# Optimization experiments

Hardware: AMD Instinct MI355X
Metric: run time of the kernel (lower is better)

Reference implementation:

```python
import jax, jax.numpy as jnp
import numpy as np

B, T, D, K = 16, 8192, 64, 1024


def setup_inputs() -> dict:
    key = jax.random.key(0)
    k1, k2 = jax.random.split(key)
    x = jax.random.normal(k1, (B, T, D, 1), dtype=jnp.float32)
    weight = jax.random.normal(k2, (K, D), dtype=jnp.float32)
    return {"x": x, "weight": weight}


def reference(x, weight):
    # x: [B, T, D, 1] -> squeeze trailing dim -> [B, T, D]
    xs = jnp.squeeze(x, axis=-1)
    x2 = jnp.sum(xs * xs, axis=-1, keepdims=True)          # [B, T, 1]
    e2 = jnp.sum(weight * weight, axis=-1)                 # [K]
    xe = jnp.einsum('btd,kd->btk', xs, weight)             # [B, T, K]
    dist2 = x2 - 2.0 * xe + e2                             # [B, T, K]
    indices = jnp.argmin(dist2, axis=-1)                   # [B, T] int
    quantized = jnp.take(weight, indices, axis=0)          # [B, T, D]
    return quantized, indices
```

## Files before the change

kernel.cpp:

```cpp
#include <hip/hip_runtime.h>

#define MTOK  131072
#define DIMD  64
#define KCODE 1024
#define TPB   256

typedef __bf16 bf16x8 __attribute__((ext_vector_type(8)));
typedef float  f32x4  __attribute__((ext_vector_type(4)));

__device__ __forceinline__ f32x4 mfma16(bf16x8 a, bf16x8 b, f32x4 c) {
    return __builtin_amdgcn_mfma_f32_16x16x32_bf16(a, b, c, 0, 0, 0);
}

__global__ __launch_bounds__(256) void prep_kernel(
    const float* __restrict__ w, __bf16* __restrict__ wpk,
    float* __restrict__ e2n, float* __restrict__ e2) {
    int b   = blockIdx.x;
    int tid = threadIdx.x;
    if (b < 64) {
        int cb  = b;
        int win = tid >> 6, lane = tid & 63;
        int q = lane >> 4, m = lane & 15;
        int k = cb * 16 + m;
        int d0 = (win & 1) * 32 + q * 8;
        const float* src = w + (size_t)k * DIMD + d0;
        float4 v0 = *(const float4*)(src);
        float4 v1 = *(const float4*)(src + 4);
        float f[8] = {v0.x, v0.y, v0.z, v0.w, v1.x, v1.y, v1.z, v1.w};
        bf16x8 o;
#pragma unroll
        for (int j = 0; j < 8; ++j) {
            __bf16 h = (__bf16)f[j];
            o[j] = (win < 2) ? h : (__bf16)(f[j] - (float)h);
        }
        *(bf16x8*)(wpk + ((size_t)(cb * 4 + win) * 64 + lane) * 8) = o;
    } else {
        int k2 = (b - 64) * 256 + tid;
        const float4* row = (const float4*)(w + (size_t)k2 * DIMD);
        float s = 0.f;
#pragma unroll
        for (int i = 0; i < 16; ++i) {
            float4 v = row[i];
            s = fmaf(v.x, v.x, s); s = fmaf(v.y, v.y, s);
            s = fmaf(v.z, v.z, s); s = fmaf(v.w, v.w, s);
        }
        e2[k2]  = s;
        e2n[k2] = -0.5f * s;
    }
}

__global__ __launch_bounds__(256, 2) void vq_main(
    const float* __restrict__ x, const float* __restrict__ wfull,
    const __bf16* __restrict__ wpk, const float* __restrict__ e2n_g,
    const float* __restrict__ e2_g, float* __restrict__ out) {

    const int tid  = threadIdx.x;
    const int blk  = blockIdx.x;
    const int lane = tid & 63;
    const int wv   = tid >> 6;
    const int q    = lane >> 4;
    const int m    = lane & 15;
    const size_t tok0 = (size_t)blk * TPB + wv * 64;

    bf16x8 bx[4][4];
#pragma unroll
    for (int tg = 0; tg < 4; ++tg) {
        const float* xr = x + (tok0 + tg * 16 + m) * DIMD;
#pragma unroll
        for (int h = 0; h < 2; ++h) {
            float4 v0 = *(const float4*)(xr + h * 32 + q * 8);
            float4 v1 = *(const float4*)(xr + h * 32 + q * 8 + 4);
            float f[8] = {v0.x, v0.y, v0.z, v0.w, v1.x, v1.y, v1.z, v1.w};
            bf16x8 hi, lo;
#pragma unroll
            for (int j = 0; j < 8; ++j) {
                __bf16 hh = (__bf16)f[j];
                hi[j] = hh;
                lo[j] = (__bf16)(f[j] - (float)hh);
            }
            bx[tg][h]     = hi;
            bx[tg][2 + h] = lo;
        }
    }

    float b1[4], b2[4]; int i1[4];
#pragma unroll
    for (int tg = 0; tg < 4; ++tg) { b1[tg] = -3e38f; b2[tg] = -3e38f; i1[tg] = 0; }

    const __bf16* wp = wpk + (size_t)lane * 8;
    const float*  ep = e2n_g + q * 4;

    auto compute = [&](const bf16x8& A0, const bf16x8& A1, const bf16x8& A2,
                       const bf16x8& A3, const f32x4& EE, int cbase) {
        __builtin_amdgcn_s_setprio(1);
        f32x4 t0 = mfma16(A0, bx[0][0], EE);
        f32x4 t1 = mfma16(A0, bx[1][0], EE);
        f32x4 t2 = mfma16(A0, bx[2][0], EE);
        f32x4 t3 = mfma16(A0, bx[3][0], EE);
        t0 = mfma16(A1, bx[0][1], t0);
        t1 = mfma16(A1, bx[1][1], t1);
        t2 = mfma16(A1, bx[2][1], t2);
        t3 = mfma16(A1, bx[3][1], t3);
        t0 = mfma16(A0, bx[0][2], t0);
        t1 = mfma16(A0, bx[1][2], t1);
        t2 = mfma16(A0, bx[2][2], t2);
        t3 = mfma16(A0, bx[3][2], t3);
        t0 = mfma16(A1, bx[0][3], t0);
        t1 = mfma16(A1, bx[1][3], t1);
        t2 = mfma16(A1, bx[2][3], t2);
        t3 = mfma16(A1, bx[3][3], t3);
        t0 = mfma16(A2, bx[0][0], t0);
        t1 = mfma16(A2, bx[1][0], t1);
        t2 = mfma16(A2, bx[2][0], t2);
        t3 = mfma16(A2, bx[3][0], t3);
        t0 = mfma16(A3, bx[0][1], t0);
        t1 = mfma16(A3, bx[1][1], t1);
        t2 = mfma16(A3, bx[2][1], t2);
        t3 = mfma16(A3, bx[3][1], t3);
        __builtin_amdgcn_s_setprio(0);
        f32x4 tt[4] = {t0, t1, t2, t3};
#pragma unroll
        for (int tg = 0; tg < 4; ++tg) {
#pragma unroll
            for (int r = 0; r < 4; ++r) {
                float a  = tt[tg][r];
                int iv   = cbase + q * 4 + r;
                bool gt  = a > b1[tg];
                i1[tg] = gt ? iv : i1[tg];
                b2[tg] = __builtin_amdgcn_fmed3f(a, b1[tg], b2[tg]);
                b1[tg] = fmaxf(a, b1[tg]);
            }
        }
    };

    bf16x8 Pa0, Pa1, Pa2, Pa3, Pb0, Pb1, Pb2, Pb3;
    f32x4  Ea, Eb;

    {
        const __bf16* wc = wp;
        Pa0 = *(const bf16x8*)(wc + 0);
        Pa1 = *(const bf16x8*)(wc + 512);
        Pa2 = *(const bf16x8*)(wc + 1024);
        Pa3 = *(const bf16x8*)(wc + 1536);
        Ea  = *(const f32x4*)(ep);
    }

    for (int cb = 0; cb < 64; cb += 2) {
        {
            const __bf16* wc = wp + (size_t)(cb + 1) * 2048;
            Pb0 = *(const bf16x8*)(wc + 0);
            Pb1 = *(const bf16x8*)(wc + 512);
            Pb2 = *(const bf16x8*)(wc + 1024);
            Pb3 = *(const bf16x8*)(wc + 1536);
            Eb  = *(const f32x4*)(ep + (cb + 1) * 16);
        }
        compute(Pa0, Pa1, Pa2, Pa3, Ea, cb * 16);
        if (cb + 2 < 64) {
            const __bf16* wc = wp + (size_t)(cb + 2) * 2048;
            Pa0 = *(const bf16x8*)(wc + 0);
            Pa1 = *(const bf16x8*)(wc + 512);
            Pa2 = *(const bf16x8*)(wc + 1024);
            Pa3 = *(const bf16x8*)(wc + 1536);
            Ea  = *(const f32x4*)(ep + (cb + 2) * 16);
        }
        compute(Pb0, Pb1, Pb2, Pb3, Eb, (cb + 1) * 16);
    }

    float B1f[4], B2f[4]; int I1f[4];
#pragma unroll
    for (int tg = 0; tg < 4; ++tg) {
        float B1 = b1[tg], B2 = b2[tg]; int I1 = i1[tg];
#pragma unroll
        for (int mask = 16; mask <= 32; mask <<= 1) {
            float ob1 = __shfl_xor(B1, mask);
            float ob2 = __shfl_xor(B2, mask);
            int   oi  = __shfl_xor(I1, mask);
            bool take = (ob1 > B1) || (ob1 == B1 && oi < I1);
            B2 = fmaxf(fminf(ob1, B1), fmaxf(ob2, B2));
            I1 = take ? oi : I1;
            B1 = fmaxf(ob1, B1);
        }
        B1f[tg] = B1; B2f[tg] = B2; I1f[tg] = I1;
    }

    int myidx;
    {
        int src = lane & 15;
        int v0 = __shfl(I1f[0], src);
        int v1 = __shfl(I1f[1], src);
        int v2 = __shfl(I1f[2], src);
        int v3 = __shfl(I1f[3], src);
        int hi2 = lane >> 4;
        int va = (hi2 & 1) ? v1 : v0;
        int vb = (hi2 & 1) ? v3 : v2;
        myidx = (hi2 & 2) ? vb : va;
    }

#pragma unroll
    for (int tg = 0; tg < 4; ++tg) {
        unsigned long long msk =
            __ballot((lane < 16) && (B1f[tg] - B2f[tg] < 2e-3f));
        while (msk) {
            int mm = __ffsll((unsigned long long)msk) - 1;
            msk &= msk - 1;
            int tloc = tg * 16 + mm;
            const float4* xr = (const float4*)(x + (tok0 + tloc) * DIMD);
            float bv = 3e38f; int bi = 0;
            for (int j = 0; j < 16; ++j) {
                int k = lane * 16 + j;
                const float4* wr = (const float4*)(wfull + (size_t)k * DIMD);
                float s = 0.f;
#pragma unroll
                for (int i = 0; i < 16; ++i) {
                    float4 xv = xr[i], wv4 = wr[i];
                    s = fmaf(xv.x, wv4.x, s); s = fmaf(xv.y, wv4.y, s);
                    s = fmaf(xv.z, wv4.z, s); s = fmaf(xv.w, wv4.w, s);
                }
                float dv = fmaf(-2.f, s, e2_g[k]);
                if (dv < bv) { bv = dv; bi = k; }
            }
#pragma unroll
            for (int mask2 = 1; mask2 <= 32; mask2 <<= 1) {
                float ov = __shfl_xor(bv, mask2);
                int   oi = __shfl_xor(bi, mask2);
                bool take = (ov < bv) || (ov == bv && oi < bi);
                bv = take ? ov : bv;
                bi = take ? oi : bi;
            }
            myidx = (lane == tloc) ? bi : myidx;
        }
    }

    __builtin_nontemporal_store((float)myidx,
                                out + (size_t)MTOK * DIMD + tok0 + lane);

    {
        float* obase = out + tok0 * DIMD;
#pragma unroll
        for (int j = 0; j < 16; ++j) {
            int srcl = j * 4 + (lane >> 4);
            int gi   = __shfl(myidx, srcl);
            f32x4 v = *(const f32x4*)(wfull + (size_t)gi * DIMD + (lane & 15) * 4);
            __builtin_nontemporal_store(v, (f32x4*)(obase + j * 256 + lane * 4));
        }
    }
}

extern "C" void kernel_launch(void* const* d_in, const int* in_sizes, int n_in,
                              void* d_out, int out_size, void* d_ws, size_t ws_size,
                              hipStream_t stream) {
    const float* x = (const float*)d_in[0];
    const float* w = (const float*)d_in[1];
    float* out = (float*)d_out;

    __bf16* wpk = (__bf16*)d_ws;
    float*  e2n = (float*)((char*)d_ws + 262144);
    float*  e2  = (float*)((char*)d_ws + 266240);

    prep_kernel<<<68, 256, 0, stream>>>(w, wpk, e2n, e2);
    vq_main<<<MTOK / TPB, 256, 0, stream>>>(x, w, wpk, e2n, e2, out);
}
```

Before: 142.9 us.

## Stage codebook chunks in LDS via double-buffered async global-to-LDS loads

Doubles the block size to 512 threads and streams the packed bf16 codebook into a double-buffered LDS tile in four 64KB chunks, using direct global-to-LDS loads. All eight waves then read the shared tile instead of each wave loading the codebook from global memory. The inner loop is also software-pipelined so the argmax tracking of one 16-code group overlaps the MFMA chain of the next. The ~132KB of LDS limits the kernel to one block per CU and adds a barrier per chunk.

```diff
diff --git a/kernel.cpp b/kernel.cpp
--- a/kernel.cpp
+++ b/kernel.cpp
@@ -3,13 +3,19 @@
 #define MTOK  131072
 #define DIMD  64
 #define KCODE 1024
-#define TPB   256
+#define TPB   512
 
 typedef __bf16 bf16x8 __attribute__((ext_vector_type(8)));
 typedef float  f32x4  __attribute__((ext_vector_type(4)));
 
 __device__ __forceinline__ f32x4 mfma16(bf16x8 a, bf16x8 b, f32x4 c) {
     return __builtin_amdgcn_mfma_f32_16x16x32_bf16(a, b, c, 0, 0, 0);
+}
+
+__device__ __forceinline__ void g2l16(const void* g, void* l) {
+    __builtin_amdgcn_global_load_lds(
+        (const __attribute__((address_space(1))) unsigned int*)g,
+        (__attribute__((address_space(3))) unsigned int*)l, 16, 0, 0);
 }
 
 __global__ __launch_bounds__(256) void prep_kernel(
@@ -49,10 +55,65 @@
     }
 }
 
-__global__ __launch_bounds__(256, 2) void vq_main(
+#define LOADW(S, WB, L)                                        \
+    W##S##0 = *(const bf16x8*)((WB) + (L) * 2048 + 0);         \
+    W##S##1 = *(const bf16x8*)((WB) + (L) * 2048 + 512);       \
+    W##S##2 = *(const bf16x8*)((WB) + (L) * 2048 + 1024);      \
+    W##S##3 = *(const bf16x8*)((WB) + (L) * 2048 + 1536);      \
+    E##S    = *(const f32x4*)&ldsE[(CB0 + (L)) * 16 + q * 4];
+
+#define CHAINS(S)                                              \
+    __builtin_amdgcn_s_setprio(1);                             \
+    t##S##0 = mfma16(W##S##0, bx[0][0], E##S);                 \
+    t##S##1 = mfma16(W##S##0, bx[1][0], E##S);                 \
+    t##S##2 = mfma16(W##S##0, bx[2][0], E##S);                 \
+    t##S##3 = mfma16(W##S##0, bx[3][0], E##S);                 \
+    t##S##0 = mfma16(W##S##1, bx[0][1], t##S##0);              \
+    t##S##1 = mfma16(W##S##1, bx[1][1], t##S##1);              \
+    t##S##2 = mfma16(W##S##1, bx[2][1], t##S##2);              \
+    t##S##3 = mfma16(W##S##1, bx[3][1], t##S##3);              \
+    t##S##0 = mfma16(W##S##0, bx[0][2], t##S##0);              \
+    t##S##1 = mfma16(W##S##0, bx[1][2], t##S##1);              \
+    t##S##2 = mfma16(W##S##0, bx[2][2], t##S##2);              \
+    t##S##3 = mfma16(W##S##0, bx[3][2], t##S##3);              \
+    t##S##0 = mfma16(W##S##1, bx[0][3], t##S##0);              \
+    t##S##1 = mfma16(W##S##1, bx[1][3], t##S##1);              \
+    t##S##2 = mfma16(W##S##1, bx[2][3], t##S##2);              \
+    t##S##3 = mfma16(W##S##1, bx[3][3], t##S##3);              \
+    t##S##0 = mfma16(W##S##2, bx[0][0], t##S##0);              \
+    t##S##1 = mfma16(W##S##2, bx[1][0], t##S##1);              \
+    t##S##2 = mfma16(W##S##2, bx[2][0], t##S##2);              \
+    t##S##3 = mfma16(W##S##2, bx[3][0], t##S##3);              \
+    t##S##0 = mfma16(W##S##3, bx[0][1], t##S##0);              \
+    t##S##1 = mfma16(W##S##3, bx[1][1], t##S##1);              \
+    t##S##2 = mfma16(W##S##3, bx[2][1], t##S##2);              \
+    t##S##3 = mfma16(W##S##3, bx[3][1], t##S##3);              \
+    __builtin_amdgcn_s_setprio(0);
+
+#define TRACK(S, CBASE)                                        \
+    {                                                          \
+        f32x4 tt_[4] = {t##S##0, t##S##1, t##S##2, t##S##3};   \
+        _Pragma("unroll")                                      \
+        for (int tg_ = 0; tg_ < 4; ++tg_) {                    \
+            _Pragma("unroll")                                  \
+            for (int r_ = 0; r_ < 4; ++r_) {                   \
+                float a_ = tt_[tg_][r_];                       \
+                int iv_  = (CBASE) + q * 4 + r_;               \
+                bool gt_ = a_ > b1[tg_];                       \
+                i1[tg_] = gt_ ? iv_ : i1[tg_];                 \
+                b2[tg_] = __builtin_amdgcn_fmed3f(a_, b1[tg_], b2[tg_]); \
+                b1[tg_] = fmaxf(a_, b1[tg_]);                  \
+            }                                                  \
+        }                                                      \
+    }
+
+__global__ __launch_bounds__(512, 2) void vq_main(
     const float* __restrict__ x, const float* __restrict__ wfull,
     const __bf16* __restrict__ wpk, const float* __restrict__ e2n_g,
     const float* __restrict__ e2_g, float* __restrict__ out) {
+
+    __shared__ __align__(16) __bf16 ldsW[2][32768];
+    __shared__ __align__(16) float  ldsE[KCODE];
 
     const int tid  = threadIdx.x;
     const int blk  = blockIdx.x;
@@ -62,6 +123,16 @@
     const int m    = lane & 15;
     const size_t tok0 = (size_t)blk * TPB + wv * 64;
 
+    {
+        const char* gw = (const char*)wpk + tid * 16;
+        char* lw = (char*)&ldsW[0][0] + tid * 16;
+#pragma unroll
+        for (int j = 0; j < 8; ++j)
+            g2l16(gw + j * 8192, lw + j * 8192);
+        if (tid < 256)
+            g2l16((const char*)e2n_g + tid * 16, (char*)ldsE + tid * 16);
+    }
+
     bf16x8 bx[4][4];
 #pragma unroll
     for (int tg = 0; tg < 4; ++tg) {
@@ -87,83 +158,41 @@
 #pragma unroll
     for (int tg = 0; tg < 4; ++tg) { b1[tg] = -3e38f; b2[tg] = -3e38f; i1[tg] = 0; }
 
-    const __bf16* wp = wpk + (size_t)lane * 8;
-    const float*  ep = e2n_g + q * 4;
-
-    auto compute = [&](const bf16x8& A0, const bf16x8& A1, const bf16x8& A2,
-                       const bf16x8& A3, const f32x4& EE, int cbase) {
-        __builtin_amdgcn_s_setprio(1);
-        f32x4 t0 = mfma16(A0, bx[0][0], EE);
-        f32x4 t1 = mfma16(A0, bx[1][0], EE);
-        f32x4 t2 = mfma16(A0, bx[2][0], EE);
-        f32x4 t3 = mfma16(A0, bx[3][0], EE);
-        t0 = mfma16(A1, bx[0][1], t0);
-        t1 = mfma16(A1, bx[1][1], t1);
-        t2 = mfma16(A1, bx[2][1], t2);
-        t3 = mfma16(A1, bx[3][1], t3);
-        t0 = mfma16(A0, bx[0][2], t0);
-        t1 = mfma16(A0, bx[1][2], t1);
-        t2 = mfma16(A0, bx[2][2], t2);
-        t3 = mfma16(A0, bx[3][2], t3);
-        t0 = mfma16(A1, bx[0][3], t0);
-        t1 = mfma16(A1, bx[1][3], t1);
-        t2 = mfma16(A1, bx[2][3], t2);
-        t3 = mfma16(A1, bx[3][3], t3);
-        t0 = mfma16(A2, bx[0][0], t0);
-        t1 = mfma16(A2, bx[1][0], t1);
-        t2 = mfma16(A2, bx[2][0], t2);
-        t3 = mfma16(A2, bx[3][0], t3);
-        t0 = mfma16(A3, bx[0][1], t0);
-        t1 = mfma16(A3, bx[1][1], t1);
-        t2 = mfma16(A3, bx[2][1], t2);
-        t3 = mfma16(A3, bx[3][1], t3);
-        __builtin_amdgcn_s_setprio(0);
-        f32x4 tt[4] = {t0, t1, t2, t3};
-#pragma unroll
-        for (int tg = 0; tg < 4; ++tg) {
-#pragma unroll
-            for (int r = 0; r < 4; ++r) {
-                float a  = tt[tg][r];
-                int iv   = cbase + q * 4 + r;
-                bool gt  = a > b1[tg];
-                i1[tg] = gt ? iv : i1[tg];
-                b2[tg] = __builtin_amdgcn_fmed3f(a, b1[tg], b2[tg]);
-                b1[tg] = fmaxf(a, b1[tg]);
-            }
-        }
-    };
-
-    bf16x8 Pa0, Pa1, Pa2, Pa3, Pb0, Pb1, Pb2, Pb3;
-    f32x4  Ea, Eb;
-
-    {
-        const __bf16* wc = wp;
-        Pa0 = *(const bf16x8*)(wc + 0);
-        Pa1 = *(const bf16x8*)(wc + 512);
-        Pa2 = *(const bf16x8*)(wc + 1024);
-        Pa3 = *(const bf16x8*)(wc + 1536);
-        Ea  = *(const f32x4*)(ep);
-    }
-
-    for (int cb = 0; cb < 64; cb += 2) {
-        {
-            const __bf16* wc = wp + (size_t)(cb + 1) * 2048;
-            Pb0 = *(const bf16x8*)(wc + 0);
-            Pb1 = *(const bf16x8*)(wc + 512);
-            Pb2 = *(const bf16x8*)(wc + 1024);
-            Pb3 = *(const bf16x8*)(wc + 1536);
-            Eb  = *(const f32x4*)(ep + (cb + 1) * 16);
-        }
-        compute(Pa0, Pa1, Pa2, Pa3, Ea, cb * 16);
-        if (cb + 2 < 64) {
-            const __bf16* wc = wp + (size_t)(cb + 2) * 2048;
-            Pa0 = *(const bf16x8*)(wc + 0);
-            Pa1 = *(const bf16x8*)(wc + 512);
-            Pa2 = *(const bf16x8*)(wc + 1024);
-            Pa3 = *(const bf16x8*)(wc + 1536);
-            Ea  = *(const f32x4*)(ep + (cb + 2) * 16);
-        }
-        compute(Pb0, Pb1, Pb2, Pb3, Eb, (cb + 1) * 16);
+    __syncthreads();
+
+    for (int ch = 0; ch < 4; ++ch) {
+        if (ch + 1 < 4) {
+            const char* gw = (const char*)wpk + (size_t)(ch + 1) * 65536 + tid * 16;
+            char* lw = (char*)&ldsW[(ch + 1) & 1][0] + tid * 16;
+#pragma unroll
+            for (int j = 0; j < 8; ++j)
+                g2l16(gw + j * 8192, lw + j * 8192);
+        }
+
+        const __bf16* wb = &ldsW[ch & 1][0] + lane * 8;
+        const int CB0 = ch * 16;
+
+        bf16x8 WA0, WA1, WA2, WA3, WB0, WB1, WB2, WB3;
+        f32x4  EA, EB, tA0, tA1, tA2, tA3, tB0, tB1, tB2, tB3;
+
+        LOADW(A, wb, 0);
+        CHAINS(A);
+
+        for (int l = 1; l <= 13; l += 2) {
+            LOADW(B, wb, l);
+            TRACK(A, (CB0 + l - 1) * 16);
+            CHAINS(B);
+            LOADW(A, wb, l + 1);
+            TRACK(B, (CB0 + l) * 16);
+            CHAINS(A);
+        }
+        LOADW(B, wb, 15);
+        TRACK(A, (CB0 + 14) * 16);
+        CHAINS(B);
+        TRACK(B, (CB0 + 15) * 16);
+
+        if (ch + 1 < 4)
+            __syncthreads();
     }
 
     float B1f[4], B2f[4]; int I1f[4];
@@ -258,5 +287,5 @@
     float*  e2  = (float*)((char*)d_ws + 266240);
 
     prep_kernel<<<68, 256, 0, stream>>>(w, wpk, e2n, e2);
-    vq_main<<<MTOK / TPB, 256, 0, stream>>>(x, w, wpk, e2n, e2, out);
-}
+    vq_main<<<MTOK / TPB, 512, 0, stream>>>(x, w, wpk, e2n, e2, out);
+}
```

After: 147.7 us. 3.4% more time.
